# Performance work log

Hardware: AMD Instinct MI355X
Metric: run time of the kernel (lower is better)

## Reference

```python
import math
import jax, jax.numpy as jnp
import numpy as np

D_MODEL = 256
N_HEADS = 8


def pos_embed_sine(h, w, num_pos_feats):
    """PositionEmbeddingSine with normalize=True; returns [2*num_pos_feats, h, w]."""
    scale = 2.0 * math.pi
    eps = 1e-6
    # cumsum of ones -> 1..h / 1..w
    y = (jnp.arange(1, h + 1, dtype=jnp.float32) - 0.5) / (h + eps) * scale
    x = (jnp.arange(1, w + 1, dtype=jnp.float32) - 0.5) / (w + eps) * scale
    i = jnp.arange(num_pos_feats, dtype=jnp.float32)
    dim_t = 10000.0 ** (2.0 * jnp.floor(i / 2.0) / num_pos_feats)
    px = x[:, None] / dim_t  # [w, F]
    py = y[:, None] / dim_t  # [h, F]

    def interleave(p):
        # stack(sin(even), cos(odd)) then flatten -> matches torch stack(...,dim=-1).flatten
        return jnp.stack([jnp.sin(p[:, 0::2]), jnp.cos(p[:, 1::2])], axis=-1).reshape(p.shape[0], -1)

    px = interleave(px)  # [w, F]
    py = interleave(py)  # [h, F]
    pos_y = jnp.broadcast_to(py[:, None, :], (h, w, num_pos_feats))
    pos_x = jnp.broadcast_to(px[None, :, :], (h, w, num_pos_feats))
    return jnp.concatenate([pos_y, pos_x], axis=-1).transpose(2, 0, 1)  # [2F, h, w]


def batched_attn_weights(q, k, Wq, bq, Wk, bk, nheads):
    """q,k: [N, S, E]. Returns head-averaged attention weights [N, L, S]
    (exactly what nn.MultiheadAttention returns with need_weights=True, eval mode)."""
    N, L, E = q.shape
    d = E // nheads
    inv = 1.0 / math.sqrt(d)
    qp = ((q @ Wq.T + bq) * inv).reshape(N, L, nheads, d).transpose(0, 2, 1, 3)   # [N,H,L,d]
    kp = (k @ Wk.T + bk).reshape(N, k.shape[1], nheads, d).transpose(0, 2, 1, 3)  # [N,H,S,d]
    scores = jnp.einsum('nhld,nhsd->nhls', qp, kp)
    w = jax.nn.softmax(scores, axis=-1)
    return w.mean(axis=1)  # average over heads -> [N,L,S]


def setup_inputs() -> dict:
    key = jax.random.key(0)
    k1, k2, k3, k4, k5 = jax.random.split(key, 5)
    x = jax.random.normal(k1, (5, D_MODEL, 80, 80), dtype=jnp.float32)
    in_proj_w = jax.random.normal(k2, (3 * D_MODEL, D_MODEL), dtype=jnp.float32) * 0.05
    in_proj_b = jax.random.normal(k3, (3 * D_MODEL,), dtype=jnp.float32) * 0.05
    sal_w = jax.random.normal(k4, (1,), dtype=jnp.float32)
    sal_b = jax.random.normal(k5, (1,), dtype=jnp.float32)
    return {"x": x, "in_proj_w": in_proj_w, "in_proj_b": in_proj_b,
            "sal_w": sal_w, "sal_b": sal_b}


def reference(x, in_proj_w, in_proj_b, sal_w, sal_b):
    b, c, h, w = x.shape  # b=5 (4 local + 1 global), c=d_model
    loc, glb = x[:4], x[4:5]
    ph, pw = h // 4, w // 4
    # 'n c (nh ph) (nw pw) -> (n nh nw) c ph pw' with nh=nw=4 -> 64 patches
    loc_p = loc.reshape(4, c, 4, ph, 4, pw).transpose(0, 2, 4, 1, 3, 5).reshape(64, c, ph, pw)
    pos = pos_embed_sine(ph, pw, c // 2)  # [c, ph, pw], identical for all patches
    query = (loc_p + pos).reshape(64, c, ph * pw).transpose(0, 2, 1)  # [64, L, c]
    # global branch: upsample x2 bilinear (align_corners=False), patch into 8x8 grid
    up_glb = jax.image.resize(glb, (1, c, 2 * h, 2 * w), method='bilinear')
    patched_glb = (up_glb.reshape(1, c, 8, ph, 8, pw)
                   .transpose(2, 4, 0, 1, 3, 5).reshape(64, c, ph, pw))
    key_t = (patched_glb + pos).reshape(64, c, ph * pw).transpose(0, 2, 1)  # [64, S, c]
    # single batched attention instead of 64 separate kernel launches
    Wq, Wk = in_proj_w[:c], in_proj_w[c:2 * c]
    bq, bk = in_proj_b[:c], in_proj_b[c:2 * c]
    aw = batched_attn_weights(query, key_t, Wq, bq, Wk, bk, N_HEADS)  # [64, L, S]
    aw_mean = aw.mean(axis=1)  # mean over query positions -> [64, S]
    # sal_conv is a 1x1 conv on a single channel == scalar affine
    imp = jax.nn.sigmoid(sal_w[0] * aw_mean.reshape(64, 1, ph, pw) + sal_b[0])
    # last_pred is None -> hist_importance initialized (torch.empty; defined here as zeros)
    current_importance = 0.6 * imp  # + 0.4 * zeros
    weighted = loc_p * current_importance  # broadcast [64,1,ph,pw]
    # '(n nh nw) c ph pw -> n c (nh ph) (nw pw)'
    loc_m = (weighted.reshape(4, 4, 4, c, ph, pw)
             .transpose(0, 3, 1, 4, 2, 5).reshape(4, c, h, w))
    # patches2image: '(hg wg b) c h w -> b c (hg h) (wg w)', hg=wg=2
    merged = (loc_m.reshape(2, 2, 1, c, h, w)
              .transpose(2, 3, 0, 4, 1, 5).reshape(1, c, 2 * h, 2 * w))
    return merged + up_glb * 0.5
```

## Files before the change

### kernel.cpp

```cpp
#include <hip/hip_runtime.h>
#include <math.h>

typedef __attribute__((ext_vector_type(8))) short bf16x8;
typedef __attribute__((ext_vector_type(8))) unsigned short u16x8;
typedef __attribute__((ext_vector_type(4))) float f32x4;
typedef unsigned short u16;


__device__ __forceinline__ u16 f2bf(float f){
  unsigned u = __float_as_uint(f);
  u += 0x7fffu + ((u >> 16) & 1u);
  return (u16)(u >> 16);
}

__device__ __forceinline__ float4 up4(const float* __restrict__ g, int Y, int X0){
  int jy = Y >> 1;
  int ry0, ry1; float wy0, wy1;
  if (Y & 1){ ry0 = jy; ry1 = (jy < 79) ? jy + 1 : 79; wy0 = 0.75f; wy1 = 0.25f; }
  else      { ry0 = (jy > 0) ? jy - 1 : 0; ry1 = jy;   wy0 = 0.25f; wy1 = 0.75f; }
  int jx = X0 >> 1;
  int cm1 = (jx > 0) ? jx - 1 : 0;
  int cp2 = (jx < 78) ? jx + 2 : 79;
  const float* r0 = g + ry0 * 80;
  const float* r1 = g + ry1 * 80;
  float cvm = wy0 * r0[cm1]  + wy1 * r1[cm1];
  float cv0 = wy0 * r0[jx]   + wy1 * r1[jx];
  float cv1 = wy0 * r0[jx+1] + wy1 * r1[jx+1];
  float cv2 = wy0 * r0[cp2]  + wy1 * r1[cp2];
  return make_float4(0.25f*cvm + 0.75f*cv0,
                     0.75f*cv0 + 0.25f*cv1,
                     0.25f*cv0 + 0.75f*cv1,
                     0.75f*cv1 + 0.25f*cv2);
}

__global__ __launch_bounds__(256) void pos_kernel(float* __restrict__ pos){
  int idx = blockIdx.x * 256 + threadIdx.x;
  int e = idx / 400, s = idx - e * 400;
  int y = s / 20, x = s - y * 20;
  int j = e & 127;
  int m = j >> 1;
  int k = (e < 128) ? y : x;
  float v = ((float)k + 0.5f) * (6.2831853071795864769f / 20.000001f);
  float invT = exp2f(-(float)m * 0.20762050593049448f);
  float arg = v * invT;
  pos[idx] = (j & 1) ? cosf(arg) : sinf(arg);
}

__global__ __launch_bounds__(256) void feat_kernel(const float* __restrict__ xin,
                                                   const float* __restrict__ pos,
                                                   u16* __restrict__ qf,
                                                   u16* __restrict__ kf){
  int which = blockIdx.y;
  int flat = blockIdx.x * 256 + threadIdx.x;
  int s4 = flat % 100;
  int rest = flat / 100;
  int e = rest & 255;
  int n = rest >> 8;
  int s0 = s4 * 4;
  int y = s0 / 20, x0 = s0 - y * 20;
  float4 pv = *(const float4*)(pos + e * 400 + s0);
  float4 val;
  u16* dst;
  if (which == 0){
    int img = n >> 4, pi = (n >> 2) & 3, pj = n & 3;
    const float* src = xin + (((img * 256 + e) * 80) + (pi * 20 + y)) * 80 + (pj * 20 + x0);
    float4 l = *(const float4*)src;
    val.x = l.x + pv.x; val.y = l.y + pv.y; val.z = l.z + pv.z; val.w = l.w + pv.w;
    dst = qf;
  } else {
    int gi = n >> 3, gj = n & 7;
    const float* g = xin + (4 * 256 + e) * 6400;
    float4 u = up4(g, gi * 20 + y, gj * 20 + x0);
    val.x = u.x + pv.x; val.y = u.y + pv.y; val.z = u.z + pv.z; val.w = u.w + pv.w;
    dst = kf;
  }
  ushort4 o;
  o.x = f2bf(val.x); o.y = f2bf(val.y); o.z = f2bf(val.z); o.w = f2bf(val.w);
  *(ushort4*)(dst + ((n * 256 + e) * 400 + s0)) = o;
}

__global__ __launch_bounds__(256) void proj_kernel(const u16* __restrict__ qf,
                                                   const u16* __restrict__ kf,
                                                   const float* __restrict__ W,
                                                   const float* __restrict__ bvec,
                                                   u16* __restrict__ qp,
                                                   u16* __restrict__ kp){
  __shared__ u16 lds_a[64 * 32];
  __shared__ u16 lds_b[400 * 32];

  int mat = blockIdx.y;
  int bx = blockIdx.x;
  int n = bx >> 2, ot = bx & 3;
  const u16* F = mat ? kf : qf;
  u16* O = mat ? kp : qp;
  const float* Wrow = W + (mat * 256 + ot * 64) * 256;
  const float* bias = bvec + mat * 256 + ot * 64;
  float scale = mat ? 1.0f : 0.25505419776f;

  int tid = threadIdx.x;
  int lane = tid & 63, wave = tid >> 6;
  int lo = lane & 15, hi = lane >> 4;

  float bl[4];
  #pragma unroll
  for (int r = 0; r < 4; r++) bl[r] = bias[wave * 16 + hi * 4 + r];

  f32x4 acc[25];
  #pragma unroll
  for (int t = 0; t < 25; t++) acc[t] = (f32x4){0.f, 0.f, 0.f, 0.f};

  for (int e0 = 0; e0 < 256; e0 += 32){
    __syncthreads();
    for (int c = tid; c < 512; c += 256){
      int row = c >> 3, e4 = c & 7;
      float4 w4 = *(const float4*)(Wrow + row * 256 + e0 + e4 * 4);
      ushort4 pk;
      pk.x = f2bf(w4.x); pk.y = f2bf(w4.y); pk.z = f2bf(w4.z); pk.w = f2bf(w4.w);
      int idx = row * 32 + ((e4 * 4) ^ ((row & 3) << 3));
      *(ushort4*)(lds_a + idx) = pk;
    }
    for (int c = tid; c < 1600; c += 256){
      int er = c & 31, s8 = c >> 5;
      u16x8 v = *(const u16x8*)(F + ((n * 256 + e0 + er) * 400 + s8 * 8));
      #pragma unroll
      for (int j = 0; j < 8; j++){
        int s = s8 * 8 + j;
        lds_b[s * 32 + (er ^ ((s & 3) << 3))] = v[j];
      }
    }
    __syncthreads();
    bf16x8 afr = *(const bf16x8*)(lds_a + (wave * 16 + lo) * 32 + ((hi * 8) ^ ((lo & 3) << 3)));
    #pragma unroll
    for (int st = 0; st < 25; st++){
      bf16x8 bfr = *(const bf16x8*)(lds_b + (st * 16 + lo) * 32 + ((hi * 8) ^ ((lo & 3) << 3)));
      acc[st] = __builtin_amdgcn_mfma_f32_16x16x32_bf16(afr, bfr, acc[st], 0, 0, 0);
    }
  }
  int o_loc = wave * 16 + hi * 4;
  int hh = ot * 2 + (o_loc >> 5);
  int d0 = o_loc & 31;
  #pragma unroll
  for (int st = 0; st < 25; st++){
    int s = st * 16 + lo;
    ushort4 pk;
    pk.x = f2bf((acc[st][0] + bl[0]) * scale);
    pk.y = f2bf((acc[st][1] + bl[1]) * scale);
    pk.z = f2bf((acc[st][2] + bl[2]) * scale);
    pk.w = f2bf((acc[st][3] + bl[3]) * scale);
    *(ushort4*)(O + ((size_t)((n * 8 + hh) * 400 + s)) * 32 + d0) = pk;
  }
}

__global__ __launch_bounds__(256) void attn_kernel(const u16* __restrict__ qp,
                                                   const u16* __restrict__ kp,
                                                   float* __restrict__ colsum2){
  __shared__ float zp[4 * 208];
  __shared__ float invzl[208];

  int bx = blockIdx.x;
  int yhalf = blockIdx.y;
  int lt0 = yhalf ? 13 : 0;
  int nl  = yhalf ? 12 : 13;
  int tid = threadIdx.x;
  int lane = tid & 63, w = tid >> 6;
  int lo = lane & 15, hi = lane >> 4;

  const u16* qb = qp + (size_t)bx * 400 * 32;
  const u16* kb = kp + (size_t)bx * 400 * 32;

  bf16x8 kfr[7];
  #pragma unroll
  for (int j = 0; j < 7; j++){
    int st = w + 4 * j;
    if (st < 25) kfr[j] = *(const bf16x8*)(kb + (st * 16 + lo) * 32 + hi * 8);
  }

  for (int li = 0; li < nl; li++){
    int lt = lt0 + li;
    bf16x8 qfr = *(const bf16x8*)(qb + (lt * 16 + lo) * 32 + hi * 8);
    float z = 0.f;
    #pragma unroll
    for (int j = 0; j < 7; j++){
      int st = w + 4 * j;
      if (st < 25){
        f32x4 sc = __builtin_amdgcn_mfma_f32_16x16x32_bf16(kfr[j], qfr, (f32x4){0.f,0.f,0.f,0.f}, 0, 0, 0);
        z += (exp2f(sc[0]) + exp2f(sc[1])) + (exp2f(sc[2]) + exp2f(sc[3]));
      }
    }
    z += __shfl_xor(z, 16, 64);
    z += __shfl_xor(z, 32, 64);
    if (hi == 0) zp[w * 208 + li * 16 + lo] = z;
  }
  __syncthreads();
  for (int i = tid; i < nl * 16; i += 256)
    invzl[i] = 1.0f / (((zp[i] + zp[208 + i]) + (zp[416 + i] + zp[624 + i])));
  __syncthreads();

  float csacc[7][4];
  #pragma unroll
  for (int j = 0; j < 7; j++){
    #pragma unroll
    for (int r = 0; r < 4; r++) csacc[j][r] = 0.f;
  }
  for (int li = 0; li < nl; li++){
    int lt = lt0 + li;
    bf16x8 qfr = *(const bf16x8*)(qb + (lt * 16 + lo) * 32 + hi * 8);
    float wl = invzl[li * 16 + lo];
    #pragma unroll
    for (int j = 0; j < 7; j++){
      int st = w + 4 * j;
      if (st < 25){
        f32x4 sc = __builtin_amdgcn_mfma_f32_16x16x32_bf16(kfr[j], qfr, (f32x4){0.f,0.f,0.f,0.f}, 0, 0, 0);
        csacc[j][0] += exp2f(sc[0]) * wl;
        csacc[j][1] += exp2f(sc[1]) * wl;
        csacc[j][2] += exp2f(sc[2]) * wl;
        csacc[j][3] += exp2f(sc[3]) * wl;
      }
    }
  }

  #pragma unroll
  for (int j = 0; j < 7; j++){
    int st = w + 4 * j;
    if (st < 25){
      #pragma unroll
      for (int r = 0; r < 4; r++){
        float v = csacc[j][r];
        v += __shfl_xor(v, 1, 64);
        v += __shfl_xor(v, 2, 64);
        v += __shfl_xor(v, 4, 64);
        v += __shfl_xor(v, 8, 64);
        if (lo == 0)
          colsum2[((size_t)(yhalf * 512 + bx)) * 400 + st * 16 + hi * 4 + r] = v;
      }
    }
  }
}

__global__ __launch_bounds__(256) void imp_kernel(const float* __restrict__ colsum2,
                                                  const float* __restrict__ sal_w,
                                                  const float* __restrict__ sal_b,
                                                  float* __restrict__ imp){
  int idx = blockIdx.x * 256 + threadIdx.x;
  int n = idx / 400, s = idx - n * 400;
  float sum = 0.f;
  #pragma unroll
  for (int h = 0; h < 8; h++){
    sum += colsum2[(size_t)(n * 8 + h) * 400 + s];
    sum += colsum2[(size_t)(512 + n * 8 + h) * 400 + s];
  }
  float aw = sum * (1.0f / 3200.0f);
  float zz = sal_w[0] * aw + sal_b[0];
  imp[idx] = 1.0f / (1.0f + __expf(-zz));
}

__global__ __launch_bounds__(256) void out_kernel(const float* __restrict__ xin,
                                                  const float* __restrict__ imp,
                                                  float* __restrict__ out){
  int flat = blockIdx.x * 256 + threadIdx.x;
  int x4 = flat % 40;
  int rest = flat / 40;
  int Y = rest % 160;
  int e = rest / 160;
  int X0 = x4 * 4;
  int a = (Y >= 80) ? 1 : 0;
  int bq = (X0 >= 80) ? 1 : 0;
  int yy = Y - a * 80, xx = X0 - bq * 80;
  int pi = yy / 20, y = yy - pi * 20;
  int pj = xx / 20, x0 = xx - pj * 20;
  int img = a * 2 + bq;
  int nn = img * 16 + pi * 4 + pj;
  int s0 = y * 20 + x0;
  float4 l4 = *(const float4*)(xin + ((img * 256 + e) * 80 + yy) * 80 + xx);
  float4 i4 = *(const float4*)(imp + nn * 400 + s0);
  const float* g = xin + (4 * 256 + e) * 6400;
  float4 u4 = up4(g, Y, X0);
  float4 o;
  o.x = l4.x * (0.6f * i4.x) + 0.5f * u4.x;
  o.y = l4.y * (0.6f * i4.y) + 0.5f * u4.y;
  o.z = l4.z * (0.6f * i4.z) + 0.5f * u4.z;
  o.w = l4.w * (0.6f * i4.w) + 0.5f * u4.w;
  *(float4*)(out + (e * 160 + Y) * 160 + X0) = o;
}

extern "C" void kernel_launch(void* const* d_in, const int* in_sizes, int n_in,
                              void* d_out, int out_size, void* d_ws, size_t ws_size,
                              hipStream_t stream) {
  const float* x      = (const float*)d_in[0];
  const float* W      = (const float*)d_in[1];
  const float* bvec   = (const float*)d_in[2];
  const float* sal_w  = (const float*)d_in[3];
  const float* sal_b  = (const float*)d_in[4];
  float* out = (float*)d_out;

  const size_t POS_OFF = 0;
  const size_t QF_OFF  = 409600;
  const size_t KF_OFF  = QF_OFF + 13107200;
  const size_t QP_OFF  = KF_OFF + 13107200;
  const size_t KP_OFF  = QP_OFF + 13107200;
  const size_t CS_OFF  = KP_OFF + 13107200;
  const size_t IMP_OFF = CS_OFF + 1638400;
  const size_t NEED    = IMP_OFF + 102400;
  if (ws_size < NEED) return;

  char* ws = (char*)d_ws;
  float* pos    = (float*)(ws + POS_OFF);
  u16*   qf     = (u16*)(ws + QF_OFF);
  u16*   kf     = (u16*)(ws + KF_OFF);
  u16*   qp     = (u16*)(ws + QP_OFF);
  u16*   kp     = (u16*)(ws + KP_OFF);
  float* colsum2= (float*)(ws + CS_OFF);
  float* imp    = (float*)(ws + IMP_OFF);

  pos_kernel<<<400, 256, 0, stream>>>(pos);
  feat_kernel<<<dim3(6400, 2), 256, 0, stream>>>(x, pos, qf, kf);
  proj_kernel<<<dim3(256, 2), 256, 0, stream>>>(qf, kf, W, bvec, qp, kp);
  attn_kernel<<<dim3(512, 2), 256, 0, stream>>>(qp, kp, colsum2);
  imp_kernel<<<100, 256, 0, stream>>>(colsum2, sal_w, sal_b, imp);
  out_kernel<<<6400, 256, 0, stream>>>(x, imp, out);
}
```

Measured before the change: 124.9 us.

## Fuse softmax two-pass into single pass with per-tile barrier and register-held probabilities

The attention kernel used to compute scores twice: one pass summed the row partition function and a second pass recomputed the MFMA and exp2 to accumulate normalized column sums. Now it keeps the exponentiated scores in registers, reduces the row sums across the four waves through a double-buffered shared array with one barrier per query tile, and accumulates right away. This removes the duplicate MFMA and exp work. In exchange it adds a __syncthreads per iteration and raises register pressure, since 28 extra floats are held live.

New measurement: 112.1 us. -10.3%, faster.

```diff
diff --git a/kernel.cpp b/kernel.cpp
--- a/kernel.cpp
+++ b/kernel.cpp
@@ -154,8 +154,7 @@
 __global__ __launch_bounds__(256) void attn_kernel(const u16* __restrict__ qp,
                                                    const u16* __restrict__ kp,
                                                    float* __restrict__ colsum2){
-  __shared__ float zp[4 * 208];
-  __shared__ float invzl[208];
+  __shared__ float zp[2][4][16];
 
   int bx = blockIdx.x;
   int yhalf = blockIdx.y;
@@ -175,46 +174,43 @@
     if (st < 25) kfr[j] = *(const bf16x8*)(kb + (st * 16 + lo) * 32 + hi * 8);
   }
 
+  float csacc[7][4];
+  #pragma unroll
+  for (int j = 0; j < 7; j++){
+    #pragma unroll
+    for (int r = 0; r < 4; r++) csacc[j][r] = 0.f;
+  }
+
   for (int li = 0; li < nl; li++){
     int lt = lt0 + li;
     bf16x8 qfr = *(const bf16x8*)(qb + (lt * 16 + lo) * 32 + hi * 8);
+    f32x4 p[7];
     float z = 0.f;
     #pragma unroll
     for (int j = 0; j < 7; j++){
       int st = w + 4 * j;
       if (st < 25){
         f32x4 sc = __builtin_amdgcn_mfma_f32_16x16x32_bf16(kfr[j], qfr, (f32x4){0.f,0.f,0.f,0.f}, 0, 0, 0);
-        z += (exp2f(sc[0]) + exp2f(sc[1])) + (exp2f(sc[2]) + exp2f(sc[3]));
+        p[j][0] = exp2f(sc[0]);
+        p[j][1] = exp2f(sc[1]);
+        p[j][2] = exp2f(sc[2]);
+        p[j][3] = exp2f(sc[3]);
+        z += (p[j][0] + p[j][1]) + (p[j][2] + p[j][3]);
       }
     }
     z += __shfl_xor(z, 16, 64);
     z += __shfl_xor(z, 32, 64);
-    if (hi == 0) zp[w * 208 + li * 16 + lo] = z;
-  }
-  __syncthreads();
-  for (int i = tid; i < nl * 16; i += 256)
-    invzl[i] = 1.0f / (((zp[i] + zp[208 + i]) + (zp[416 + i] + zp[624 + i])));
-  __syncthreads();
-
-  float csacc[7][4];
-  #pragma unroll
-  for (int j = 0; j < 7; j++){
-    #pragma unroll
-    for (int r = 0; r < 4; r++) csacc[j][r] = 0.f;
-  }
-  for (int li = 0; li < nl; li++){
-    int lt = lt0 + li;
-    bf16x8 qfr = *(const bf16x8*)(qb + (lt * 16 + lo) * 32 + hi * 8);
-    float wl = invzl[li * 16 + lo];
+    int par = li & 1;
+    if (hi == 0) zp[par][w][lo] = z;
+    __syncthreads();
+    float invz = 1.0f / ((zp[par][0][lo] + zp[par][1][lo]) + (zp[par][2][lo] + zp[par][3][lo]));
     #pragma unroll
     for (int j = 0; j < 7; j++){
-      int st = w + 4 * j;
-      if (st < 25){
-        f32x4 sc = __builtin_amdgcn_mfma_f32_16x16x32_bf16(kfr[j], qfr, (f32x4){0.f,0.f,0.f,0.f}, 0, 0, 0);
-        csacc[j][0] += exp2f(sc[0]) * wl;
-        csacc[j][1] += exp2f(sc[1]) * wl;
-        csacc[j][2] += exp2f(sc[2]) * wl;
-        csacc[j][3] += exp2f(sc[3]) * wl;
+      if (w + 4 * j < 25){
+        csacc[j][0] += p[j][0] * invz;
+        csacc[j][1] += p[j][1] * invz;
+        csacc[j][2] += p[j][2] * invz;
+        csacc[j][3] += p[j][3] * invz;
       }
     }
   }
```
